# Performance work log

Hardware: AMD Instinct MI355X
Metric: run time of the kernel (lower is better)

Reference implementation:

```python
import jax, jax.numpy as jnp
import numpy as np

B, N, D = 2, 512, 256
H, HD = 4, 64  # hidden_dim=256 split across 4 heads (is_concat=True)
SLOPE = 0.2


def setup_inputs() -> dict:
    key = jax.random.key(0)
    ks = jax.random.split(key, 8)
    rn = lambda k, sh: jax.random.normal(k, sh, dtype=jnp.float32)
    return {
        "query": rn(ks[0], (B, N, D)),
        "key_in": rn(ks[1], (B, N, D)),
        "value": rn(ks[2], (B, N, D)),
        "w_q": rn(ks[3], (D, H * HD)) * 0.05,  # shared query/key projection (share_weights=True)
        "b_q": rn(ks[4], (H * HD,)) * 0.05,
        "w_v": rn(ks[5], (D, H * HD)) * 0.05,
        "b_v": rn(ks[6], (H * HD,)) * 0.05,
        "a": rn(ks[7], (HD,)) * 0.05,  # attention Linear(hd, 1, bias=False), shared across heads
    }


def reference(query, key_in, value, w_q, b_q, w_v, b_v, a):
    hq = (query @ w_q + b_q).reshape(B, N, H, HD)
    hk = (key_in @ w_q + b_q).reshape(B, N, H, HD)  # share_weights=True
    hv = (value @ w_v + b_v).reshape(B, N, H, HD)
    # torch repeat/repeat_interleave + view gives h[b,i,j] = hq[b,j] + hk[b,i]
    h = hq[:, None, :, :, :] + hk[:, :, None, :, :]  # [B, N, N, H, HD]
    e = jnp.einsum('bijhf,f->bijh', jax.nn.leaky_relu(h, SLOPE), a)
    e = jax.nn.softmax(e, axis=2)  # softmax over source nodes j (dropout is identity in eval)
    out = jnp.einsum('bijh,bjhf->bihf', e, hv).reshape(B, N, H * HD)  # is_concat
    h_prime = jax.nn.relu(out)
    return h_prime, e
```

## Files before the change

kernel.cpp:

```cpp
#include <hip/hip_runtime.h>


#define NB 2
#define NN 512
#define DD 256
#define NH 4
#define HDIM 64

typedef __attribute__((ext_vector_type(2))) float f32x2;

__device__ __forceinline__ float rl(float v, int u) {
    return __uint_as_float(__builtin_amdgcn_readlane(__float_as_uint(v), u));
}
__device__ __forceinline__ f32x2 pk_fma(f32x2 a, f32x2 b, f32x2 c) {
    return __builtin_elementwise_fma(a, b, c);
}
__device__ __forceinline__ f32x2 pk_abs(f32x2 t) {
    return __builtin_elementwise_max(t, -t);
}

__global__ __launch_bounds__(256, 4) void proj_kernel(
    const float* __restrict__ q, const float* __restrict__ kin, const float* __restrict__ vin,
    const float* __restrict__ wq, const float* __restrict__ bq,
    const float* __restrict__ wv, const float* __restrict__ bv,
    float* __restrict__ hq, float* __restrict__ hk, float* __restrict__ hv)
{
    const int m = blockIdx.z;
    const float* x    = (m == 0) ? q  : (m == 1) ? kin : vin;
    const float* w    = (m == 2) ? wv : wq;
    const float* bias = (m == 2) ? bv : bq;
    float* out        = (m == 0) ? hq : (m == 1) ? hk : hv;

    const int r0 = blockIdx.x * 16;
    const int cb = blockIdx.y * 128;
    const int t  = threadIdx.x;

    __shared__ float xs[16][DD + 4];

    #pragma unroll
    for (int p = 0; p < 4; ++p) {
        const int idx = t + 256 * p;
        const int row = idx >> 6;
        const int kc  = idx & 63;
        const float4 v = *reinterpret_cast<const float4*>(&x[(size_t)(r0 + row) * DD + kc * 4]);
        *reinterpret_cast<float4*>(&xs[row][kc * 4]) = v;
    }
    __syncthreads();

    const int row0 = (t >> 5) * 2;
    const int c0   = (t & 31) * 4;

    const float4 b4 = *reinterpret_cast<const float4*>(&bias[cb + c0]);
    float acc[2][4];
    #pragma unroll
    for (int r = 0; r < 2; ++r) { acc[r][0]=b4.x; acc[r][1]=b4.y; acc[r][2]=b4.z; acc[r][3]=b4.w; }

    for (int kt = 0; kt < DD; kt += 4) {
        const float4 a0 = *reinterpret_cast<const float4*>(&xs[row0][kt]);
        const float4 a1 = *reinterpret_cast<const float4*>(&xs[row0 + 1][kt]);
        const float xa0[4] = {a0.x, a0.y, a0.z, a0.w};
        const float xa1[4] = {a1.x, a1.y, a1.z, a1.w};
        #pragma unroll
        for (int kk = 0; kk < 4; ++kk) {
            const float4 w4 = *reinterpret_cast<const float4*>(&w[(size_t)(kt + kk) * DD + cb + c0]);
            const float wv4[4] = {w4.x, w4.y, w4.z, w4.w};
            #pragma unroll
            for (int c = 0; c < 4; ++c) {
                acc[0][c] = fmaf(xa0[kk], wv4[c], acc[0][c]);
                acc[1][c] = fmaf(xa1[kk], wv4[c], acc[1][c]);
            }
        }
    }
    #pragma unroll
    for (int r = 0; r < 2; ++r) {
        float4 o; o.x = acc[r][0]; o.y = acc[r][1]; o.z = acc[r][2]; o.w = acc[r][3];
        *reinterpret_cast<float4*>(&out[(size_t)(r0 + row0 + r) * DD + cb + c0]) = o;
    }
}

__global__ __launch_bounds__(512, 8) void attn_kernel(
    const float* __restrict__ hq, const float* __restrict__ hk, const float* __restrict__ hv,
    const float* __restrict__ a, float* __restrict__ out_hp, float* __restrict__ out_e)
{
    const int t   = threadIdx.x;
    const int b   = blockIdx.x >> 9;
    const int rem = blockIdx.x & 511;
    const int i0  = (rem >> 2) * 4;
    const int h   = rem & 3;

    __shared__ float s[4][NN + 8];
    __shared__ float part[8][4][HDIM];

    const float* hk0 = hk + ((size_t)(b * NN) + i0) * DD + h * HDIM;

    {
        const int j = t;
        const float* qbase = hq + ((size_t)(b * NN) + j) * DD + h * HDIM;
        f32x2 accu = {0.f, 0.f};
        f32x2 acc[4] = {};
        #pragma unroll
        for (int fc = 0; fc < 16; ++fc) {
            const int fo = fc * 4;
            const float4 q4 = *reinterpret_cast<const float4*>(qbase + fo);
            const float4 a4 = *reinterpret_cast<const float4*>(a + fo);
            const f32x2 av[2] = {{a4.x, a4.y}, {a4.z, a4.w}};
            const f32x2 qv[2] = {{q4.x, q4.y}, {q4.z, q4.w}};
            #pragma unroll
            for (int ii = 0; ii < 4; ++ii) {
                const float4 kv = *reinterpret_cast<const float4*>(hk0 + ii * DD + fo);
                const f32x2 kk0 = {kv.x, kv.y}, kk1 = {kv.z, kv.w};
                acc[ii] = pk_fma(pk_abs(qv[0] + kk0), av[0], acc[ii]);
                acc[ii] = pk_fma(pk_abs(qv[1] + kk1), av[1], acc[ii]);
            }
            accu = pk_fma(qv[0], av[0], accu);
            accu = pk_fma(qv[1], av[1], accu);
        }
        const float su = 0.6f * (accu.x + accu.y);
        #pragma unroll
        for (int ii = 0; ii < 4; ++ii)
            s[ii][j] = fmaf(0.4f, acc[ii].x + acc[ii].y, su);
    }
    __syncthreads();

    {
        const int wv = t >> 6, lane = t & 63;
        if (wv < 4) {
            float* row = &s[wv][0];
            float vals[8]; float mx = -1e30f;
            #pragma unroll
            for (int k2 = 0; k2 < 8; ++k2) { vals[k2] = row[lane + 64 * k2]; mx = fmaxf(mx, vals[k2]); }
            #pragma unroll
            for (int off = 32; off; off >>= 1) mx = fmaxf(mx, __shfl_xor(mx, off, 64));
            float sum = 0.f;
            #pragma unroll
            for (int k2 = 0; k2 < 8; ++k2) { vals[k2] = __expf(vals[k2] - mx); sum += vals[k2]; }
            #pragma unroll
            for (int off = 32; off; off >>= 1) sum += __shfl_xor(sum, off, 64);
            const float inv = 1.0f / sum;
            #pragma unroll
            for (int k2 = 0; k2 < 8; ++k2) row[lane + 64 * k2] = vals[k2] * inv;
        }
    }
    __syncthreads();

    {
        float* oe = out_e + (((size_t)(b * NN) + i0) * NN) * NH + h;
        #pragma unroll
        for (int k2 = 0; k2 < 4; ++k2) {
            const int idx = t + 512 * k2;
            const int ii = idx >> 9;
            const int j  = idx & 511;
            oe[((size_t)ii * NN + j) * NH] = s[ii][j];
        }
    }

    {
        const int col  = t & 63;
        const int jg   = t >> 6;
        const int lane = t & 63;
        const int jbase = jg * 64;
        f32x2 acc2[4] = {};
        const float* hvb = hv + (size_t)(b * NN) * DD + h * HDIM + col;
        const float e0 = s[0][jbase + lane];
        const float e1 = s[1][jbase + lane];
        const float e2 = s[2][jbase + lane];
        const float e3 = s[3][jbase + lane];
        #pragma unroll
        for (int ub = 0; ub < 4; ++ub) {
            float hvv[16];
            #pragma unroll
            for (int k = 0; k < 16; ++k)
                hvv[k] = hvb[(size_t)(jbase + ub * 16 + k) * DD];
            #pragma unroll
            for (int k = 0; k < 16; k += 2) {
                const int u = ub * 16 + k;
                const f32x2 hv2 = {hvv[k], hvv[k + 1]};
                acc2[0] = pk_fma(f32x2{rl(e0, u), rl(e0, u + 1)}, hv2, acc2[0]);
                acc2[1] = pk_fma(f32x2{rl(e1, u), rl(e1, u + 1)}, hv2, acc2[1]);
                acc2[2] = pk_fma(f32x2{rl(e2, u), rl(e2, u + 1)}, hv2, acc2[2]);
                acc2[3] = pk_fma(f32x2{rl(e3, u), rl(e3, u + 1)}, hv2, acc2[3]);
            }
        }
        #pragma unroll
        for (int ii = 0; ii < 4; ++ii) part[jg][ii][col] = acc2[ii].x + acc2[ii].y;
    }
    __syncthreads();
    if (t < 256) {
        const int ii = t >> 6, col = t & 63;
        float v = 0.f;
        #pragma unroll
        for (int jg = 0; jg < 8; ++jg) v += part[jg][ii][col];
        out_hp[((size_t)(b * NN) + i0 + ii) * DD + h * HDIM + col] = v > 0.f ? v : 0.f;
    }
}

extern "C" void kernel_launch(void* const* d_in, const int* in_sizes, int n_in,
                              void* d_out, int out_size, void* d_ws, size_t ws_size,
                              hipStream_t stream) {
    const float* q   = (const float*)d_in[0];
    const float* kin = (const float*)d_in[1];
    const float* vin = (const float*)d_in[2];
    const float* wq  = (const float*)d_in[3];
    const float* bq  = (const float*)d_in[4];
    const float* wv  = (const float*)d_in[5];
    const float* bv  = (const float*)d_in[6];
    const float* a   = (const float*)d_in[7];

    float* out_hp = (float*)d_out;
    float* out_e  = out_hp + (size_t)NB * NN * DD;

    float* hq = (float*)d_ws;
    float* hk = hq + (size_t)NB * NN * DD;
    float* hv = hk + (size_t)NB * NN * DD;

    proj_kernel<<<dim3(64, 2, 3), 256, 0, stream>>>(q, kin, vin, wq, bq, wv, bv, hq, hk, hv);
    attn_kernel<<<dim3(NB * 128 * NH), 512, 0, stream>>>(hq, hk, hv, a, out_hp, out_e);
}
```

Before: 121.4 us.

## Restructure e·V accumulation to use float4 V loads and LDS-broadcast weights

The attention-times-value stage changes its thread mapping. Each lane now loads a float4 of V covering four columns for one of four j sub-rows, and reads the softmax weights from shared memory. This replaces scalar strided V loads and per-element readlane broadcasts. The partial-sum buffer grows fourfold to hold the per-jsub partials, and the final reduction sums 32 partials instead of 8. It trades readlane SALU traffic and narrow global loads for more LDS reads and a larger reduction.

```diff
diff --git a/kernel.cpp b/kernel.cpp
--- a/kernel.cpp
+++ b/kernel.cpp
@@ -9,9 +9,6 @@
 
 typedef __attribute__((ext_vector_type(2))) float f32x2;
 
-__device__ __forceinline__ float rl(float v, int u) {
-    return __uint_as_float(__builtin_amdgcn_readlane(__float_as_uint(v), u));
-}
 __device__ __forceinline__ f32x2 pk_fma(f32x2 a, f32x2 b, f32x2 c) {
     return __builtin_elementwise_fma(a, b, c);
 }
@@ -89,7 +86,7 @@
     const int h   = rem & 3;
 
     __shared__ float s[4][NN + 8];
-    __shared__ float part[8][4][HDIM];
+    __shared__ float part[8][4][4][HDIM];
 
     const float* hk0 = hk + ((size_t)(b * NN) + i0) * DD + h * HDIM;
 
@@ -155,41 +152,43 @@
     }
 
     {
-        const int col  = t & 63;
-        const int jg   = t >> 6;
+        const int w    = t >> 6;
         const int lane = t & 63;
-        const int jbase = jg * 64;
-        f32x2 acc2[4] = {};
-        const float* hvb = hv + (size_t)(b * NN) * DD + h * HDIM + col;
-        const float e0 = s[0][jbase + lane];
-        const float e1 = s[1][jbase + lane];
-        const float e2 = s[2][jbase + lane];
-        const float e3 = s[3][jbase + lane];
-        #pragma unroll
-        for (int ub = 0; ub < 4; ++ub) {
-            float hvv[16];
-            #pragma unroll
-            for (int k = 0; k < 16; ++k)
-                hvv[k] = hvb[(size_t)(jbase + ub * 16 + k) * DD];
-            #pragma unroll
-            for (int k = 0; k < 16; k += 2) {
-                const int u = ub * 16 + k;
-                const f32x2 hv2 = {hvv[k], hvv[k + 1]};
-                acc2[0] = pk_fma(f32x2{rl(e0, u), rl(e0, u + 1)}, hv2, acc2[0]);
-                acc2[1] = pk_fma(f32x2{rl(e1, u), rl(e1, u + 1)}, hv2, acc2[1]);
-                acc2[2] = pk_fma(f32x2{rl(e2, u), rl(e2, u + 1)}, hv2, acc2[2]);
-                acc2[3] = pk_fma(f32x2{rl(e3, u), rl(e3, u + 1)}, hv2, acc2[3]);
+        const int jsub = lane >> 4;
+        const int c0   = (lane & 15) * 4;
+        const int jbase = w * 64;
+        f32x2 acc0[4], acc1[4];
+        #pragma unroll
+        for (int ii = 0; ii < 4; ++ii) { acc0[ii] = f32x2{0.f, 0.f}; acc1[ii] = f32x2{0.f, 0.f}; }
+        const float* hvb = hv + (size_t)(b * NN) * DD + h * HDIM + c0;
+        #pragma unroll
+        for (int it = 0; it < 16; ++it) {
+            const int j = jbase + it * 4 + jsub;
+            const float4 v4 = *reinterpret_cast<const float4*>(hvb + (size_t)j * DD);
+            const f32x2 v0 = {v4.x, v4.y}, v1 = {v4.z, v4.w};
+            #pragma unroll
+            for (int ii = 0; ii < 4; ++ii) {
+                const float e = s[ii][j];
+                const f32x2 e2 = {e, e};
+                acc0[ii] = pk_fma(e2, v0, acc0[ii]);
+                acc1[ii] = pk_fma(e2, v1, acc1[ii]);
             }
         }
         #pragma unroll
-        for (int ii = 0; ii < 4; ++ii) part[jg][ii][col] = acc2[ii].x + acc2[ii].y;
+        for (int ii = 0; ii < 4; ++ii) {
+            float4 o; o.x = acc0[ii].x; o.y = acc0[ii].y; o.z = acc1[ii].x; o.w = acc1[ii].y;
+            *reinterpret_cast<float4*>(&part[w][jsub][ii][c0]) = o;
+        }
     }
     __syncthreads();
     if (t < 256) {
         const int ii = t >> 6, col = t & 63;
         float v = 0.f;
         #pragma unroll
-        for (int jg = 0; jg < 8; ++jg) v += part[jg][ii][col];
+        for (int w = 0; w < 8; ++w)
+            #pragma unroll
+            for (int js = 0; js < 4; ++js)
+                v += part[w][js][ii][col];
         out_hp[((size_t)(b * NN) + i0 + ii) * DD + h * HDIM + col] = v > 0.f ? v : 0.f;
     }
 }
```

Result: faster. 118.0 us (-2.8%).
